# Kernel optimization log

Measured on AMD Instinct MI355X. Metric: run time of the kernel, lower is better.

Reference implementation:

```python
import jax, jax.numpy as jnp
import numpy as np
from jax import lax

DIM = 256


def _lstm_scan(x_tbd, lengths, W, b, c0, h0):
    """Masked LSTM over time. x_tbd: [T,B,D]. CudnnCompatible gate order i,g,f,o, forget_bias=0.
    Returns final (c, h) with states frozen at t >= lengths (dynamic_rnn semantics)."""
    T = x_tbd.shape[0]

    def step(carry, inp):
        c, h = carry
        xt, t = inp
        gates = jnp.concatenate([xt, h], axis=-1) @ W + b  # [B, 4D]
        i, g, f, o = jnp.split(gates, 4, axis=-1)
        c_new = jax.nn.sigmoid(f) * c + jax.nn.sigmoid(i) * jnp.tanh(g)
        h_new = jnp.tanh(c_new) * jax.nn.sigmoid(o)
        mask = (t < lengths)[:, None]
        c = jnp.where(mask, c_new, c)
        h = jnp.where(mask, h_new, h)
        y = jnp.where(mask, h_new, jnp.zeros_like(h_new))
        return (c, h), y

    (c, h), ys = lax.scan(step, (c0, h0), (x_tbd, jnp.arange(T)))
    return c, h, ys


def _reverse_seq(x, lengths):
    """tf.reverse_sequence along time axis 1: reverse first lengths[b] steps, keep the rest."""
    T = x.shape[1]
    t = jnp.arange(T)[None, :]
    L = lengths[:, None]
    idx = jnp.where(t < L, L - 1 - t, t)  # [B, T]
    return jnp.take_along_axis(x, idx[:, :, None], axis=1)


def setup_inputs() -> dict:
    key = jax.random.key(0)
    ks = jax.random.split(key, 12)
    B, T, D = 64, 512, DIM
    x = jax.random.normal(ks[0], (B, T, D), dtype=jnp.float32)
    length = jax.random.randint(ks[1], (B,), 1, T + 1, dtype=jnp.int32)
    scale = 1.0 / np.sqrt(2 * D)
    W_f = jax.random.normal(ks[2], (2 * D, 4 * D), dtype=jnp.float32) * scale
    b_f = jnp.zeros((4 * D,), dtype=jnp.float32)
    W_b = jax.random.normal(ks[3], (2 * D, 4 * D), dtype=jnp.float32) * scale
    b_b = jnp.zeros((4 * D,), dtype=jnp.float32)
    c_init_f = jax.random.normal(ks[4], (1, D), dtype=jnp.float32) * 0.01
    h_init_f = jax.random.normal(ks[5], (1, D), dtype=jnp.float32) * 0.01
    c_init_b = jax.random.normal(ks[6], (1, D), dtype=jnp.float32) * 0.01
    h_init_b = jax.random.normal(ks[7], (1, D), dtype=jnp.float32) * 0.01
    W_fc = jax.random.normal(ks[8], (2 * D, D), dtype=jnp.float32) * (1.0 / np.sqrt(2 * D))
    return {"x": x, "length": length, "W_f": W_f, "b_f": b_f, "W_b": W_b, "b_b": b_b,
            "c_init_f": c_init_f, "h_init_f": h_init_f, "c_init_b": c_init_b,
            "h_init_b": h_init_b, "W_fc": W_fc}


def reference(x, length, W_f, b_f, W_b, b_b, c_init_f, h_init_f, c_init_b, h_init_b, W_fc):
    B = x.shape[0]
    c0_f = jnp.tile(c_init_f, (B, 1))
    h0_f = jnp.tile(h_init_f, (B, 1))
    c0_b = jnp.tile(c_init_b, (B, 1))
    h0_b = jnp.tile(h_init_b, (B, 1))
    x_tbd = jnp.swapaxes(x, 0, 1)  # [T,B,D]
    _, h_f, _ = _lstm_scan(x_tbd, length, W_f, b_f, c0_f, h0_f)
    x_rev = jnp.swapaxes(_reverse_seq(x, length), 0, 1)
    _, h_b, _ = _lstm_scan(x_rev, length, W_b, b_b, c0_b, h0_b)
    # return_seq=False: concat final hidden states and project (no bias)
    return jnp.concatenate([h_f, h_b], axis=-1) @ W_fc
```

## Files before the change

kernel.cpp:

```cpp
#include <hip/hip_runtime.h>

#define T_STEPS 512
#define BATCH   64
#define DIMS    256
#define NBLK    16
#define NDIR    2

typedef short bf16x8 __attribute__((ext_vector_type(8)));
typedef float f32x4  __attribute__((ext_vector_type(4)));
typedef unsigned int u32x4 __attribute__((ext_vector_type(4)));

__device__ __forceinline__ unsigned short f2bf(float f) {
  union { float f; unsigned int u; } v; v.f = f;
  unsigned int b = v.u;
  return (unsigned short)((b + 0x7FFFu + ((b >> 16) & 1u)) >> 16);
}

__device__ __forceinline__ float sigm(float x) {
  return __builtin_amdgcn_rcpf(1.0f + __builtin_amdgcn_exp2f(-1.44269504f * x));
}
__device__ __forceinline__ float tanh_(float x) {
  return 1.0f - 2.0f * __builtin_amdgcn_rcpf(1.0f + __builtin_amdgcn_exp2f(2.88539008f * x));
}

__device__ __forceinline__ f32x4 bcast4(float s) {
  f32x4 v; v[0] = s; v[1] = s; v[2] = s; v[3] = s; return v;
}

__global__ void prep_x(const float* __restrict__ x, unsigned short* __restrict__ xbf) {
  size_t i = ((size_t)blockIdx.x * 256 + threadIdx.x) * 4;
  const float4 v = *reinterpret_cast<const float4*>(x + i);
  uint2 o;
  o.x = (unsigned)f2bf(v.x) | ((unsigned)f2bf(v.y) << 16);
  o.y = (unsigned)f2bf(v.z) | ((unsigned)f2bf(v.w) << 16);
  *reinterpret_cast<uint2*>(xbf + i) = o;
}

__global__ void prep_w(const float* __restrict__ Wf, const float* __restrict__ Wb,
                       unsigned short* __restrict__ WT) {
  int d = blockIdx.x >> 10, col = blockIdx.x & 1023;
  const float* W = d ? Wb : Wf;
  int k = threadIdx.x;
  WT[((size_t)(d * 1024 + col)) * 512 + k] = f2bf(W[(size_t)k * 1024 + col]);
}

__global__ __launch_bounds__(256, 1) void lstm_rec(
    const unsigned short* __restrict__ xbf,
    const unsigned short* __restrict__ WT,
    const float* __restrict__ bias_f, const float* __restrict__ bias_b,
    const float* __restrict__ ci_f, const float* __restrict__ hi_f,
    const float* __restrict__ ci_b, const float* __restrict__ hi_b,
    const int* __restrict__ length,
    unsigned int* hbuf,
    float* hfinal)
{
  const int blk = blockIdx.x;
  const int d = blk >> 4, g = blk & 15;
  const int lane = threadIdx.x & 63;
  const int wv = threadIdx.x >> 6;
  const int lhi = lane >> 4, llo = lane & 15;

  const float* bias = d ? bias_b : bias_f;
  const float* cini = d ? ci_b : ci_f;
  const float* hini = d ? hi_b : hi_f;
  unsigned int* hb = hbuf + (size_t)d * (2 * BATCH * DIMS);

  const int dim = g * 16 + llo;

  bf16x8 wf[4][16];
  #pragma unroll
  for (int gate = 0; gate < 4; ++gate) {
    #pragma unroll
    for (int ks = 0; ks < 16; ++ks) {
      const unsigned short* p =
          WT + ((size_t)(d * 1024 + gate * 256 + dim)) * 512 + ks * 32 + lhi * 8;
      wf[gate][ks] = *reinterpret_cast<const bf16x8*>(p);
      asm volatile("" : "+v"(wf[gate][ks]));
    }
  }
  float bs[4];
  #pragma unroll
  for (int gate = 0; gate < 4; ++gate) bs[gate] = bias[gate * 256 + dim];

  const int b0 = wv * 16 + lhi * 4;
  float c[4], h[4];
  int Ld[4];
  #pragma unroll
  for (int j = 0; j < 4; ++j) {
    c[j] = cini[dim]; h[j] = hini[dim]; Ld[j] = length[b0 + j];
  }

  const int bx = wv * 16 + llo;
  const int Lx = length[bx];

  #pragma unroll
  for (int j = 0; j < 4; ++j) {
    unsigned int val = (1u << 16) | (unsigned int)f2bf(h[j]);
    const unsigned int* ap = hb + (b0 + j) * DIMS + dim;
    asm volatile("global_store_dword %0, %1, off sc0 sc1"
                 :: "v"(ap), "v"(val) : "memory");
  }

  bf16x8 xa[8];
  {
    const int tx0 = (d == 0) ? 0 : (Lx - 1);
    const unsigned short* xp = xbf + ((size_t)bx * T_STEPS + tx0) * DIMS + lhi * 8;
    #pragma unroll
    for (int ks = 0; ks < 8; ++ks) xa[ks] = *reinterpret_cast<const bf16x8*>(xp + ks * 32);
  }

  #pragma unroll 1
  for (int t = 0; t < T_STEPS; ++t) {
    f32x4 acc[4];
    #pragma unroll
    for (int gate = 0; gate < 4; ++gate) acc[gate] = bcast4(bs[gate]);

    #pragma unroll
    for (int ks = 0; ks < 8; ++ks) {
      #pragma unroll
      for (int gate = 0; gate < 4; ++gate)
        acc[gate] = __builtin_amdgcn_mfma_f32_16x16x32_bf16(xa[ks], wf[gate][ks], acc[gate], 0, 0, 0);
    }

    const unsigned int* hr = hb + (size_t)(t & 1) * (BATCH * DIMS) + bx * DIMS + lhi * 8;
    u32x4 w[16];
    {
      const unsigned int tagsh = (unsigned int)(t + 1) << 16;
      bool ready;
      do {
        #pragma unroll
        for (int ks = 0; ks < 8; ++ks) {
          const unsigned int* p = hr + ks * 32;
          asm volatile("global_load_dwordx4 %0, %1, off sc0 sc1"
                       : "=v"(w[2 * ks]) : "v"(p) : "memory");
          asm volatile("global_load_dwordx4 %0, %1, off sc0 sc1"
                       : "=v"(w[2 * ks + 1]) : "v"(p + 4) : "memory");
        }
        asm volatile("s_waitcnt vmcnt(0)" ::: "memory");
        unsigned int bad = 0;
        #pragma unroll
        for (int i = 0; i < 16; ++i)
          #pragma unroll
          for (int q = 0; q < 4; ++q)
            bad |= (w[i][q] ^ tagsh);
        ready = ((bad >> 16) == 0);
      } while (!__all(ready));
    }
    __builtin_amdgcn_sched_barrier(0);

    bf16x8 ha[8];
    #pragma unroll
    for (int ks = 0; ks < 8; ++ks) {
      union { bf16x8 v; unsigned int dd[4]; } u;
      u.dd[0] = (w[2 * ks][0]     & 0xFFFFu) | (w[2 * ks][1]     << 16);
      u.dd[1] = (w[2 * ks][2]     & 0xFFFFu) | (w[2 * ks][3]     << 16);
      u.dd[2] = (w[2 * ks + 1][0] & 0xFFFFu) | (w[2 * ks + 1][1] << 16);
      u.dd[3] = (w[2 * ks + 1][2] & 0xFFFFu) | (w[2 * ks + 1][3] << 16);
      ha[ks] = u.v;
    }

    if (t + 1 < T_STEPS) {
      const int tn = t + 1;
      const int tx = (d == 0) ? tn : ((tn < Lx) ? (Lx - 1 - tn) : tn);
      const unsigned short* xp = xbf + ((size_t)bx * T_STEPS + tx) * DIMS + lhi * 8;
      #pragma unroll
      for (int ks = 0; ks < 8; ++ks) xa[ks] = *reinterpret_cast<const bf16x8*>(xp + ks * 32);
    }

    #pragma unroll
    for (int ks = 0; ks < 8; ++ks) {
      #pragma unroll
      for (int gate = 0; gate < 4; ++gate)
        acc[gate] = __builtin_amdgcn_mfma_f32_16x16x32_bf16(ha[ks], wf[gate][ks + 8], acc[gate], 0, 0, 0);
    }

    unsigned int* hw = hb + (size_t)((t + 1) & 1) * (BATCH * DIMS);
    const unsigned int ptag = (unsigned int)(t + 2) << 16;
    #pragma unroll
    for (int j = 0; j < 4; ++j) {
      const float gi = acc[0][j], gg = acc[1][j], gf = acc[2][j], go = acc[3][j];
      const float cn = sigm(gf) * c[j] + sigm(gi) * tanh_(gg);
      const float hn = tanh_(cn) * sigm(go);
      if (t < Ld[j]) { c[j] = cn; h[j] = hn; }
      unsigned int val = ptag | (unsigned int)f2bf(h[j]);
      const unsigned int* ap = hw + (b0 + j) * DIMS + dim;
      asm volatile("global_store_dword %0, %1, off sc0 sc1"
                   :: "v"(ap), "v"(val) : "memory");
    }
  }

  #pragma unroll
  for (int j = 0; j < 4; ++j)
    hfinal[((size_t)d * BATCH + b0 + j) * DIMS + dim] = h[j];
}

__global__ void final_gemm(const float* __restrict__ hfinal, const float* __restrict__ Wfc,
                           float* __restrict__ out) {
  __shared__ float hrow[512];
  const int b = blockIdx.x, col = threadIdx.x;
  hrow[col]       = hfinal[(size_t)b * DIMS + col];
  hrow[256 + col] = hfinal[(size_t)(BATCH + b) * DIMS + col];
  __syncthreads();
  float acc = 0.f;
  #pragma unroll 8
  for (int k = 0; k < 512; ++k) acc = fmaf(hrow[k], Wfc[(size_t)k * DIMS + col], acc);
  out[(size_t)b * DIMS + col] = acc;
}

extern "C" void kernel_launch(void* const* d_in, const int* in_sizes, int n_in,
                              void* d_out, int out_size, void* d_ws, size_t ws_size,
                              hipStream_t stream) {
  const float* x        = (const float*)d_in[0];
  const int*   length   = (const int*)d_in[1];
  const float* W_f      = (const float*)d_in[2];
  const float* b_f      = (const float*)d_in[3];
  const float* W_b      = (const float*)d_in[4];
  const float* b_b      = (const float*)d_in[5];
  const float* c_init_f = (const float*)d_in[6];
  const float* h_init_f = (const float*)d_in[7];
  const float* c_init_b = (const float*)d_in[8];
  const float* h_init_b = (const float*)d_in[9];
  const float* W_fc     = (const float*)d_in[10];
  float* out = (float*)d_out;

  char* ws = (char*)d_ws;
  unsigned short* xbf = (unsigned short*)(ws);
  unsigned short* WT  = (unsigned short*)(ws + 16777216);
  unsigned int*   hbf = (unsigned int*)(ws + 16777216 + 2097152);
  float* hfinal       = (float*)(ws + 16777216 + 2097152 + 524288);

  hipMemsetAsync(hbf, 0, NDIR * 2 * BATCH * DIMS * sizeof(unsigned int), stream);
  prep_x<<<8192, 256, 0, stream>>>(x, xbf);
  prep_w<<<2048, 512, 0, stream>>>(W_f, W_b, WT);
  lstm_rec<<<NBLK * NDIR, 256, 0, stream>>>(xbf, WT, b_f, b_b,
                                            c_init_f, h_init_f, c_init_b, h_init_b,
                                            length, hbf, hfinal);
  final_gemm<<<BATCH, 256, 0, stream>>>(hfinal, W_fc, out);
}
```

Measured before the change: 2.094 ms.

## Add per-wave progress counters to gate h polling before reading tagged data

```diff
diff --git a/kernel.cpp b/kernel.cpp
--- a/kernel.cpp
+++ b/kernel.cpp
@@ -52,7 +52,8 @@
     const float* __restrict__ ci_b, const float* __restrict__ hi_b,
     const int* __restrict__ length,
     unsigned int* hbuf,
-    float* hfinal)
+    float* hfinal,
+    int* cnt)
 {
   const int blk = blockIdx.x;
   const int d = blk >> 4, g = blk & 15;
@@ -64,6 +65,7 @@
   const float* cini = d ? ci_b : ci_f;
   const float* hini = d ? hi_b : hi_f;
   unsigned int* hb = hbuf + (size_t)d * (2 * BATCH * DIMS);
+  int* cl = cnt + (d * 4 + wv) * 16;
 
   const int dim = g * 16 + llo;
 
@@ -100,6 +102,13 @@
     asm volatile("global_store_dword %0, %1, off sc0 sc1"
                  :: "v"(ap), "v"(val) : "memory");
   }
+  asm volatile("s_waitcnt vmcnt(0)" ::: "memory");
+  if (lane == 0) {
+    int one = 1;
+    const int* ap = cl + g;
+    asm volatile("global_store_dword %0, %1, off sc0 sc1"
+                 :: "v"(ap), "v"(one) : "memory");
+  }
 
   bf16x8 xa[8];
   {
@@ -120,6 +129,21 @@
       #pragma unroll
       for (int gate = 0; gate < 4; ++gate)
         acc[gate] = __builtin_amdgcn_mfma_f32_16x16x32_bf16(xa[ks], wf[gate][ks], acc[gate], 0, 0, 0);
+    }
+
+    {
+      const int* cp = cl + (lane & 15);
+      bool ok;
+      unsigned int spins = 0;
+      do {
+        int v;
+        asm volatile("global_load_dword %0, %1, off sc0 sc1"
+                     : "=v"(v) : "v"(cp) : "memory");
+        asm volatile("s_waitcnt vmcnt(0)" ::: "memory");
+        __builtin_amdgcn_sched_barrier(0);
+        ok = (v >= t + 1);
+        if (++spins > (1u << 22)) ok = true;
+      } while (!__all(ok));
     }
 
     const unsigned int* hr = hb + (size_t)(t & 1) * (BATCH * DIMS) + bx * DIMS + lhi * 8;
@@ -127,6 +151,7 @@
     {
       const unsigned int tagsh = (unsigned int)(t + 1) << 16;
       bool ready;
+      unsigned int spins = 0;
       do {
         #pragma unroll
         for (int ks = 0; ks < 8; ++ks) {
@@ -137,6 +162,7 @@
                        : "=v"(w[2 * ks + 1]) : "v"(p + 4) : "memory");
         }
         asm volatile("s_waitcnt vmcnt(0)" ::: "memory");
+        __builtin_amdgcn_sched_barrier(0);
         unsigned int bad = 0;
         #pragma unroll
         for (int i = 0; i < 16; ++i)
@@ -144,6 +170,7 @@
           for (int q = 0; q < 4; ++q)
             bad |= (w[i][q] ^ tagsh);
         ready = ((bad >> 16) == 0);
+        if (++spins > (1u << 16)) ready = true;
       } while (!__all(ready));
     }
     __builtin_amdgcn_sched_barrier(0);
@@ -186,6 +213,14 @@
       const unsigned int* ap = hw + (b0 + j) * DIMS + dim;
       asm volatile("global_store_dword %0, %1, off sc0 sc1"
                    :: "v"(ap), "v"(val) : "memory");
+    }
+
+    asm volatile("s_waitcnt vmcnt(0)" ::: "memory");
+    if (lane == 0) {
+      int nv = t + 2;
+      const int* ap = cl + g;
+      asm volatile("global_store_dword %0, %1, off sc0 sc1"
+                   :: "v"(ap), "v"(nv) : "memory");
     }
   }
 
@@ -227,13 +262,14 @@
   unsigned short* xbf = (unsigned short*)(ws);
   unsigned short* WT  = (unsigned short*)(ws + 16777216);
   unsigned int*   hbf = (unsigned int*)(ws + 16777216 + 2097152);
-  float* hfinal       = (float*)(ws + 16777216 + 2097152 + 524288);
-
-  hipMemsetAsync(hbf, 0, NDIR * 2 * BATCH * DIMS * sizeof(unsigned int), stream);
+  int*   cnt          = (int*)(ws + 16777216 + 2097152 + 524288);
+  float* hfinal       = (float*)(ws + 16777216 + 2097152 + 524288 + 4096);
+
+  hipMemsetAsync(hbf, 0, 524288 + 4096, stream);
   prep_x<<<8192, 256, 0, stream>>>(x, xbf);
   prep_w<<<2048, 512, 0, stream>>>(W_f, W_b, WT);
   lstm_rec<<<NBLK * NDIR, 256, 0, stream>>>(xbf, WT, b_f, b_b,
                                             c_init_f, h_init_f, c_init_b, h_init_b,
-                                            length, hbf, hfinal);
+                                            length, hbf, hfinal, cnt);
   final_gemm<<<BATCH, 256, 0, stream>>>(hfinal, W_fc, out);
 }
```

After: 2.419 ms. 1.16x slower.

## Precompute input projections with a parallel GEMM and run recurrence per batch-group with LDS sync

Applied to the files above, without the earlier changes.

```diff
diff --git a/kernel.cpp b/kernel.cpp
--- a/kernel.cpp
+++ b/kernel.cpp
@@ -3,7 +3,6 @@
 #define T_STEPS 512
 #define BATCH   64
 #define DIMS    256
-#define NBLK    16
 #define NDIR    2
 
 typedef short bf16x8 __attribute__((ext_vector_type(8)));
@@ -15,16 +14,212 @@
   unsigned int b = v.u;
   return (unsigned short)((b + 0x7FFFu + ((b >> 16) & 1u)) >> 16);
 }
-
+__device__ __forceinline__ float bf2f(unsigned short s) {
+  union { unsigned int u; float f; } v; v.u = ((unsigned int)s) << 16; return v.f;
+}
 __device__ __forceinline__ float sigm(float x) {
   return __builtin_amdgcn_rcpf(1.0f + __builtin_amdgcn_exp2f(-1.44269504f * x));
 }
 __device__ __forceinline__ float tanh_(float x) {
   return 1.0f - 2.0f * __builtin_amdgcn_rcpf(1.0f + __builtin_amdgcn_exp2f(2.88539008f * x));
 }
-
 __device__ __forceinline__ f32x4 bcast4(float s) {
   f32x4 v; v[0] = s; v[1] = s; v[2] = s; v[3] = s; return v;
+}
+
+__global__ void prep_w(const float* __restrict__ Wf, const float* __restrict__ Wb,
+                       unsigned short* __restrict__ WT) {
+  int d = blockIdx.x >> 10, col = blockIdx.x & 1023;
+  const float* W = d ? Wb : Wf;
+  int k = threadIdx.x;
+  WT[((size_t)(d * 1024 + col)) * 512 + k] = f2bf(W[(size_t)k * 1024 + col]);
+}
+
+__global__ __launch_bounds__(512, 1) void gx_gemm(
+    const float* __restrict__ x, const int* __restrict__ length,
+    const unsigned short* __restrict__ WT,
+    const float* __restrict__ bias_f, const float* __restrict__ bias_b,
+    unsigned short* __restrict__ Gx)
+{
+  __shared__ unsigned char Alds[65536];
+  const int bid = blockIdx.x;
+  const int d = bid >> 11, mt = (bid >> 3) & 255, nt = bid & 7;
+  const int tid = threadIdx.x;
+  const float* bias = d ? bias_b : bias_f;
+
+  {
+    const int r = tid >> 2, q = tid & 3;
+    const int m = mt * 128 + r;
+    const int b = m >> 9, t = m & 511;
+    const int L = length[b];
+    const int tx = (d == 0) ? t : ((t < L) ? (L - 1 - t) : t);
+    const float* xp = x + ((size_t)b * 512 + tx) * 256 + q * 64;
+    #pragma unroll
+    for (int i = 0; i < 8; ++i) {
+      const float4 v0 = *reinterpret_cast<const float4*>(xp + i * 8);
+      const float4 v1 = *reinterpret_cast<const float4*>(xp + i * 8 + 4);
+      union { bf16x8 v; unsigned short s[8]; } u;
+      u.s[0] = f2bf(v0.x); u.s[1] = f2bf(v0.y); u.s[2] = f2bf(v0.z); u.s[3] = f2bf(v0.w);
+      u.s[4] = f2bf(v1.x); u.s[5] = f2bf(v1.y); u.s[6] = f2bf(v1.z); u.s[7] = f2bf(v1.w);
+      const int byte = (r * 512 + (q * 64 + i * 8) * 2) ^ ((r & 7) << 4);
+      *reinterpret_cast<bf16x8*>(&Alds[byte]) = u.v;
+    }
+  }
+  __syncthreads();
+
+  const int lane = tid & 63, wv = tid >> 6;
+  const int lhi = lane >> 4, llo = lane & 15;
+
+  f32x4 acc[8];
+  #pragma unroll
+  for (int tc = 0; tc < 8; ++tc) acc[tc] = bcast4(bias[nt * 128 + tc * 16 + llo]);
+
+  #pragma unroll
+  for (int kf = 0; kf < 8; ++kf) {
+    const int row = 16 * wv + llo;
+    const int abyte = (row * 512 + (kf * 32 + lhi * 8) * 2) ^ ((row & 7) << 4);
+    const bf16x8 af = *reinterpret_cast<const bf16x8*>(&Alds[abyte]);
+    #pragma unroll
+    for (int tc = 0; tc < 8; ++tc) {
+      const unsigned short* bp =
+          WT + ((size_t)(d * 1024 + nt * 128 + tc * 16 + llo)) * 512 + kf * 32 + lhi * 8;
+      const bf16x8 bf = *reinterpret_cast<const bf16x8*>(bp);
+      acc[tc] = __builtin_amdgcn_mfma_f32_16x16x32_bf16(af, bf, acc[tc], 0, 0, 0);
+    }
+  }
+
+  #pragma unroll
+  for (int tc = 0; tc < 8; ++tc) {
+    #pragma unroll
+    for (int j = 0; j < 4; ++j) {
+      const int m = mt * 128 + 16 * wv + lhi * 4 + j;
+      Gx[((size_t)(d * 32768 + m)) * 1024 + nt * 128 + tc * 16 + llo] = f2bf(acc[tc][j]);
+    }
+  }
+}
+
+__global__ __launch_bounds__(512, 1) void lstm_rec2(
+    const unsigned short* __restrict__ WT,
+    const unsigned short* __restrict__ Gx,
+    const float* __restrict__ ci_f, const float* __restrict__ hi_f,
+    const float* __restrict__ ci_b, const float* __restrict__ hi_b,
+    const int* __restrict__ length,
+    float* __restrict__ hfinal)
+{
+  __shared__ unsigned char hlds[2][8192];
+  const int d = blockIdx.x >> 2, q = blockIdx.x & 3;
+  const int tid = threadIdx.x, lane = tid & 63, wv = tid >> 6;
+  const int lhi = lane >> 4, llo = lane & 15;
+  const float* cini = d ? ci_b : ci_f;
+  const float* hini = d ? hi_b : hi_f;
+
+  bf16x8 wf[8][8];
+  #pragma unroll
+  for (int tc = 0; tc < 8; ++tc) {
+    const int gc = (tc >> 1) * 256 + wv * 32 + (tc & 1) * 16 + llo;
+    #pragma unroll
+    for (int kf = 0; kf < 8; ++kf) {
+      const unsigned short* p =
+          WT + ((size_t)(d * 1024 + gc)) * 512 + 256 + kf * 32 + lhi * 8;
+      wf[tc][kf] = *reinterpret_cast<const bf16x8*>(p);
+      asm volatile("" : "+v"(wf[tc][kf]));
+    }
+  }
+
+  float c[2][4], h[2][4];
+  int Ld[4];
+  #pragma unroll
+  for (int j = 0; j < 4; ++j) Ld[j] = length[q * 16 + lhi * 4 + j];
+  #pragma unroll
+  for (int hf = 0; hf < 2; ++hf) {
+    const int dim = wv * 32 + hf * 16 + llo;
+    #pragma unroll
+    for (int j = 0; j < 4; ++j) { c[hf][j] = cini[dim]; h[hf][j] = hini[dim]; }
+  }
+
+  #pragma unroll
+  for (int hf = 0; hf < 2; ++hf) {
+    const int dim = wv * 32 + hf * 16 + llo;
+    #pragma unroll
+    for (int j = 0; j < 4; ++j) {
+      const int row = lhi * 4 + j;
+      const int byte = (row * 512 + dim * 2) ^ ((row & 7) << 4);
+      *reinterpret_cast<unsigned short*>(&hlds[0][byte]) = f2bf(h[hf][j]);
+    }
+  }
+  __syncthreads();
+
+  const unsigned short* gxb[4];
+  #pragma unroll
+  for (int j = 0; j < 4; ++j)
+    gxb[j] = Gx + ((size_t)(d * 64 + q * 16 + lhi * 4 + j)) * 512 * 1024 + wv * 32 + llo;
+
+  unsigned short gxp[8][4];
+  #pragma unroll
+  for (int tc = 0; tc < 8; ++tc) {
+    const int off = (tc >> 1) * 256 + (tc & 1) * 16;
+    #pragma unroll
+    for (int j = 0; j < 4; ++j) gxp[tc][j] = gxb[j][off];
+  }
+
+  int cur = 0;
+  #pragma unroll 1
+  for (int t = 0; t < T_STEPS; ++t) {
+    f32x4 acc[8];
+    #pragma unroll
+    for (int tc = 0; tc < 8; ++tc)
+      #pragma unroll
+      for (int j = 0; j < 4; ++j) acc[tc][j] = bf2f(gxp[tc][j]);
+
+    if (t + 1 < T_STEPS) {
+      #pragma unroll
+      for (int tc = 0; tc < 8; ++tc) {
+        const int off = (tc >> 1) * 256 + (tc & 1) * 16 + 1024;
+        #pragma unroll
+        for (int j = 0; j < 4; ++j) gxp[tc][j] = gxb[j][off];
+      }
+    }
+    #pragma unroll
+    for (int j = 0; j < 4; ++j) gxb[j] += 1024;
+
+    bf16x8 ha[8];
+    #pragma unroll
+    for (int kf = 0; kf < 8; ++kf) {
+      const int byte = (llo * 512 + (kf * 32 + lhi * 8) * 2) ^ ((llo & 7) << 4);
+      ha[kf] = *reinterpret_cast<const bf16x8*>(&hlds[cur][byte]);
+    }
+    #pragma unroll
+    for (int kf = 0; kf < 8; ++kf)
+      #pragma unroll
+      for (int tc = 0; tc < 8; ++tc)
+        acc[tc] = __builtin_amdgcn_mfma_f32_16x16x32_bf16(ha[kf], wf[tc][kf], acc[tc], 0, 0, 0);
+
+    #pragma unroll
+    for (int hf = 0; hf < 2; ++hf) {
+      const int dim = wv * 32 + hf * 16 + llo;
+      #pragma unroll
+      for (int j = 0; j < 4; ++j) {
+        const float gi = acc[0 + hf][j], gg = acc[2 + hf][j];
+        const float gf = acc[4 + hf][j], go = acc[6 + hf][j];
+        const float cn = sigm(gf) * c[hf][j] + sigm(gi) * tanh_(gg);
+        const float hn = tanh_(cn) * sigm(go);
+        if (t < Ld[j]) { c[hf][j] = cn; h[hf][j] = hn; }
+        const int row = lhi * 4 + j;
+        const int byte = (row * 512 + dim * 2) ^ ((row & 7) << 4);
+        *reinterpret_cast<unsigned short*>(&hlds[cur ^ 1][byte]) = f2bf(h[hf][j]);
+      }
+    }
+    __syncthreads();
+    cur ^= 1;
+  }
+
+  #pragma unroll
+  for (int hf = 0; hf < 2; ++hf) {
+    const int dim = wv * 32 + hf * 16 + llo;
+    #pragma unroll
+    for (int j = 0; j < 4; ++j)
+      hfinal[((size_t)(d * 64 + q * 16 + lhi * 4 + j)) * 256 + dim] = h[hf][j];
+  }
 }
 
 __global__ void prep_x(const float* __restrict__ x, unsigned short* __restrict__ xbf) {
@@ -36,40 +231,28 @@
   *reinterpret_cast<uint2*>(xbf + i) = o;
 }
 
-__global__ void prep_w(const float* __restrict__ Wf, const float* __restrict__ Wb,
-                       unsigned short* __restrict__ WT) {
-  int d = blockIdx.x >> 10, col = blockIdx.x & 1023;
-  const float* W = d ? Wb : Wf;
-  int k = threadIdx.x;
-  WT[((size_t)(d * 1024 + col)) * 512 + k] = f2bf(W[(size_t)k * 1024 + col]);
-}
-
-__global__ __launch_bounds__(256, 1) void lstm_rec(
-    const unsigned short* __restrict__ xbf,
-    const unsigned short* __restrict__ WT,
+__global__ __launch_bounds__(256, 1) void lstm_rec_fb(
+    const unsigned short* __restrict__ xbf, const unsigned short* __restrict__ WT,
     const float* __restrict__ bias_f, const float* __restrict__ bias_b,
     const float* __restrict__ ci_f, const float* __restrict__ hi_f,
     const float* __restrict__ ci_b, const float* __restrict__ hi_b,
     const int* __restrict__ length,
-    unsigned int* hbuf,
-    float* hfinal)
+    unsigned int* hbuf, float* hfinal)
 {
   const int blk = blockIdx.x;
   const int d = blk >> 4, g = blk & 15;
   const int lane = threadIdx.x & 63;
   const int wv = threadIdx.x >> 6;
   const int lhi = lane >> 4, llo = lane & 15;
-
   const float* bias = d ? bias_b : bias_f;
   const float* cini = d ? ci_b : ci_f;
   const float* hini = d ? hi_b : hi_f;
   unsigned int* hb = hbuf + (size_t)d * (2 * BATCH * DIMS);
-
   const int dim = g * 16 + llo;
 
   bf16x8 wf[4][16];
   #pragma unroll
-  for (int gate = 0; gate < 4; ++gate) {
+  for (int gate = 0; gate < 4; ++gate)
     #pragma unroll
     for (int ks = 0; ks < 16; ++ks) {
       const unsigned short* p =
@@ -77,19 +260,14 @@
       wf[gate][ks] = *reinterpret_cast<const bf16x8*>(p);
       asm volatile("" : "+v"(wf[gate][ks]));
     }
-  }
   float bs[4];
   #pragma unroll
   for (int gate = 0; gate < 4; ++gate) bs[gate] = bias[gate * 256 + dim];
 
   const int b0 = wv * 16 + lhi * 4;
-  float c[4], h[4];
-  int Ld[4];
-  #pragma unroll
-  for (int j = 0; j < 4; ++j) {
-    c[j] = cini[dim]; h[j] = hini[dim]; Ld[j] = length[b0 + j];
-  }
-
+  float c[4], h[4]; int Ld[4];
+  #pragma unroll
+  for (int j = 0; j < 4; ++j) { c[j] = cini[dim]; h[j] = hini[dim]; Ld[j] = length[b0 + j]; }
   const int bx = wv * 16 + llo;
   const int Lx = length[bx];
 
@@ -97,8 +275,7 @@
   for (int j = 0; j < 4; ++j) {
     unsigned int val = (1u << 16) | (unsigned int)f2bf(h[j]);
     const unsigned int* ap = hb + (b0 + j) * DIMS + dim;
-    asm volatile("global_store_dword %0, %1, off sc0 sc1"
-                 :: "v"(ap), "v"(val) : "memory");
+    asm volatile("global_store_dword %0, %1, off sc0 sc1" :: "v"(ap), "v"(val) : "memory");
   }
 
   bf16x8 xa[8];
@@ -114,36 +291,32 @@
     f32x4 acc[4];
     #pragma unroll
     for (int gate = 0; gate < 4; ++gate) acc[gate] = bcast4(bs[gate]);
-
-    #pragma unroll
-    for (int ks = 0; ks < 8; ++ks) {
+    #pragma unroll
+    for (int ks = 0; ks < 8; ++ks)
       #pragma unroll
       for (int gate = 0; gate < 4; ++gate)
         acc[gate] = __builtin_amdgcn_mfma_f32_16x16x32_bf16(xa[ks], wf[gate][ks], acc[gate], 0, 0, 0);
-    }
 
     const unsigned int* hr = hb + (size_t)(t & 1) * (BATCH * DIMS) + bx * DIMS + lhi * 8;
     u32x4 w[16];
     {
       const unsigned int tagsh = (unsigned int)(t + 1) << 16;
-      bool ready;
+      bool ready; unsigned int spins = 0;
       do {
         #pragma unroll
         for (int ks = 0; ks < 8; ++ks) {
           const unsigned int* p = hr + ks * 32;
-          asm volatile("global_load_dwordx4 %0, %1, off sc0 sc1"
-                       : "=v"(w[2 * ks]) : "v"(p) : "memory");
-          asm volatile("global_load_dwordx4 %0, %1, off sc0 sc1"
-                       : "=v"(w[2 * ks + 1]) : "v"(p + 4) : "memory");
+          asm volatile("global_load_dwordx4 %0, %1, off sc0 sc1" : "=v"(w[2*ks]) : "v"(p) : "memory");
+          asm volatile("global_load_dwordx4 %0, %1, off sc0 sc1" : "=v"(w[2*ks+1]) : "v"(p + 4) : "memory");
         }
         asm volatile("s_waitcnt vmcnt(0)" ::: "memory");
         unsigned int bad = 0;
         #pragma unroll
         for (int i = 0; i < 16; ++i)
           #pragma unroll
-          for (int q = 0; q < 4; ++q)
-            bad |= (w[i][q] ^ tagsh);
+          for (int qq = 0; qq < 4; ++qq) bad |= (w[i][qq] ^ tagsh);
         ready = ((bad >> 16) == 0);
+        if (++spins > (1u << 20)) ready = true;
       } while (!__all(ready));
     }
     __builtin_amdgcn_sched_barrier(0);
@@ -152,13 +325,12 @@
     #pragma unroll
     for (int ks = 0; ks < 8; ++ks) {
       union { bf16x8 v; unsigned int dd[4]; } u;
-      u.dd[0] = (w[2 * ks][0]     & 0xFFFFu) | (w[2 * ks][1]     << 16);
-      u.dd[1] = (w[2 * ks][2]     & 0xFFFFu) | (w[2 * ks][3]     << 16);
-      u.dd[2] = (w[2 * ks + 1][0] & 0xFFFFu) | (w[2 * ks + 1][1] << 16);
-      u.dd[3] = (w[2 * ks + 1][2] & 0xFFFFu) | (w[2 * ks + 1][3] << 16);
+      u.dd[0] = (w[2*ks][0]   & 0xFFFFu) | (w[2*ks][1]   << 16);
+      u.dd[1] = (w[2*ks][2]   & 0xFFFFu) | (w[2*ks][3]   << 16);
+      u.dd[2] = (w[2*ks+1][0] & 0xFFFFu) | (w[2*ks+1][1] << 16);
+      u.dd[3] = (w[2*ks+1][2] & 0xFFFFu) | (w[2*ks+1][3] << 16);
       ha[ks] = u.v;
     }
-
     if (t + 1 < T_STEPS) {
       const int tn = t + 1;
       const int tx = (d == 0) ? tn : ((tn < Lx) ? (Lx - 1 - tn) : tn);
@@ -166,13 +338,11 @@
       #pragma unroll
       for (int ks = 0; ks < 8; ++ks) xa[ks] = *reinterpret_cast<const bf16x8*>(xp + ks * 32);
     }
-
-    #pragma unroll
-    for (int ks = 0; ks < 8; ++ks) {
+    #pragma unroll
+    for (int ks = 0; ks < 8; ++ks)
       #pragma unroll
       for (int gate = 0; gate < 4; ++gate)
         acc[gate] = __builtin_amdgcn_mfma_f32_16x16x32_bf16(ha[ks], wf[gate][ks + 8], acc[gate], 0, 0, 0);
-    }
 
     unsigned int* hw = hb + (size_t)((t + 1) & 1) * (BATCH * DIMS);
     const unsigned int ptag = (unsigned int)(t + 2) << 16;
@@ -184,11 +354,9 @@
       if (t < Ld[j]) { c[j] = cn; h[j] = hn; }
       unsigned int val = ptag | (unsigned int)f2bf(h[j]);
       const unsigned int* ap = hw + (b0 + j) * DIMS + dim;
-      asm volatile("global_store_dword %0, %1, off sc0 sc1"
-                   :: "v"(ap), "v"(val) : "memory");
-    }
-  }
-
+      asm volatile("global_store_dword %0, %1, off sc0 sc1" :: "v"(ap), "v"(val) : "memory");
+    }
+  }
   #pragma unroll
   for (int j = 0; j < 4; ++j)
     hfinal[((size_t)d * BATCH + b0 + j) * DIMS + dim] = h[j];
@@ -222,18 +390,35 @@
   const float* h_init_b = (const float*)d_in[9];
   const float* W_fc     = (const float*)d_in[10];
   float* out = (float*)d_out;
-
   char* ws = (char*)d_ws;
-  unsigned short* xbf = (unsigned short*)(ws);
-  unsigned short* WT  = (unsigned short*)(ws + 16777216);
-  unsigned int*   hbf = (unsigned int*)(ws + 16777216 + 2097152);
-  float* hfinal       = (float*)(ws + 16777216 + 2097152 + 524288);
-
-  hipMemsetAsync(hbf, 0, NDIR * 2 * BATCH * DIMS * sizeof(unsigned int), stream);
-  prep_x<<<8192, 256, 0, stream>>>(x, xbf);
-  prep_w<<<2048, 512, 0, stream>>>(W_f, W_b, WT);
-  lstm_rec<<<NBLK * NDIR, 256, 0, stream>>>(xbf, WT, b_f, b_b,
-                                            c_init_f, h_init_f, c_init_b, h_init_b,
-                                            length, hbf, hfinal);
-  final_gemm<<<BATCH, 256, 0, stream>>>(hfinal, W_fc, out);
-}
+
+  const size_t WT_SZ = 2097152;
+  const size_t GX_SZ = 134217728;
+  const size_t HF_SZ = 131072;
+  const size_t FAST_NEED = WT_SZ + GX_SZ + HF_SZ;
+
+  if (ws_size >= FAST_NEED) {
+    unsigned short* WT  = (unsigned short*)(ws);
+    unsigned short* Gx  = (unsigned short*)(ws + WT_SZ);
+    float* hfinal       = (float*)(ws + WT_SZ + GX_SZ);
+
+    prep_w<<<2048, 512, 0, stream>>>(W_f, W_b, WT);
+    gx_gemm<<<4096, 512, 0, stream>>>(x, length, WT, b_f, b_b, Gx);
+    lstm_rec2<<<8, 512, 0, stream>>>(WT, Gx, c_init_f, h_init_f, c_init_b, h_init_b,
+                                     length, hfinal);
+    final_gemm<<<BATCH, 256, 0, stream>>>(hfinal, W_fc, out);
+  } else {
+    unsigned short* xbf = (unsigned short*)(ws);
+    unsigned short* WT  = (unsigned short*)(ws + 16777216);
+    unsigned int*   hbf = (unsigned int*)(ws + 16777216 + 2097152);
+    float* hfinal       = (float*)(ws + 16777216 + 2097152 + 524288);
+
+    hipMemsetAsync(hbf, 0, NDIR * 2 * BATCH * DIMS * sizeof(unsigned int), stream);
+    prep_x<<<8192, 256, 0, stream>>>(x, xbf);
+    prep_w<<<2048, 512, 0, stream>>>(W_f, W_b, WT);
+    lstm_rec_fb<<<32, 256, 0, stream>>>(xbf, WT, b_f, b_b,
+                                        c_init_f, h_init_f, c_init_b, h_init_b,
+                                        length, hbf, hfinal);
+    final_gemm<<<BATCH, 256, 0, stream>>>(hfinal, W_fc, out);
+  }
+}
```

Measured after the change: 4.794 ms. 129% more time.
